# Performance work log

Measured on AMD Instinct MI355X. Metric: run time of the kernel, lower is better.

The kernel has to match this reference:

```python
import jax, jax.numpy as jnp
import numpy as np

B, C_IN, H, W = 2, 32, 512, 512
HIDDEN, SIZE = 768, 16
LATENT, NUM_CLASS = 128, 21
HP, WP = H // SIZE, W // SIZE
EPS = 1e-8
TEMP = 0.5


def setup_inputs() -> dict:
    key = jax.random.key(0)
    k1, k2, k3, k4, k5 = jax.random.split(key, 5)
    x = jax.random.normal(k1, (B, C_IN, H, W), dtype=jnp.float32)
    mask = jax.random.randint(k2, (B, NUM_CLASS, HP, WP), 0, 2).astype(jnp.int32)
    conv_w = jax.random.normal(k3, (HIDDEN, C_IN, SIZE, SIZE), dtype=jnp.float32) * 0.02
    conv_b = jax.random.normal(k4, (HIDDEN,), dtype=jnp.float32) * 0.02
    latent = jax.random.normal(k5, (1, LATENT * NUM_CLASS, HIDDEN), dtype=jnp.float32)
    return {"x": x, "mask": mask, "conv_w": conv_w, "conv_b": conv_b, "latent": latent}


def reference(x, mask, conv_w, conv_b, latent):
    # Patch embedding: Conv2d(kernel=stride=16) -> (B, HIDDEN, HP, WP)
    patch = jax.lax.conv_general_dilated(
        x, conv_w, window_strides=(SIZE, SIZE), padding='VALID',
        dimension_numbers=('NCHW', 'OIHW', 'NCHW'))
    patch = patch + conv_b[None, :, None, None]
    Bv = x.shape[0]
    N = HP * WP
    patch = patch.reshape(Bv, HIDDEN, N).transpose(0, 2, 1)  # (B, N, D)
    lat = jnp.broadcast_to(latent, (Bv, LATENT * NUM_CLASS, HIDDEN))  # (B, LC, D)

    # Cosine similarity as normalized batched matmul (same math as
    # torch CosineSimilarity over broadcast (B, LC, N, D))
    dots = jnp.einsum('bld,bnd->bln', lat, patch)  # (B, LC, N)
    lat_norm = jnp.linalg.norm(lat, axis=-1)       # (B, LC)
    pat_norm = jnp.linalg.norm(patch, axis=-1)     # (B, N)
    sim = dots / jnp.maximum(lat_norm[:, :, None] * pat_norm[:, None, :], EPS)

    sim = sim.reshape(Bv, LATENT, NUM_CLASS, HP, WP).mean(axis=1)  # (B, C, HP, WP)

    m = mask.astype(jnp.float32) >= 0.5
    s = jnp.sum(jnp.where(m, jnp.exp(sim / TEMP), 0.0))
    return -jnp.log(s)
```

## Files before the change

kernel.cpp:

```cpp
#include <hip/hip_runtime.h>
#include <hip/hip_bf16.h>
#include <math.h>

#define B_     2
#define CIN    32
#define HH     512
#define WW     512
#define HID    768
#define SZ     16
#define NPATCH 1024
#define KDIM   8192
#define NCLS   21
#define LAT    128
#define LC     2688
#define NP     (B_ * NPATCH)

typedef __attribute__((ext_vector_type(8))) short short8;
typedef __attribute__((ext_vector_type(4))) float f32x4;

__device__ __forceinline__ ushort f2bf(float f) {
    union { float f; unsigned u; } v; v.f = f;
    unsigned r = (v.u + 0x7fff + ((v.u >> 16) & 1)) >> 16;
    return (ushort)r;
}
__device__ __forceinline__ float bf2f(ushort u) {
    union { unsigned u; float f; } v; v.u = (unsigned)u << 16;
    return v.f;
}

__device__ __forceinline__ void gload16(const void* g, void* l) {
    __builtin_amdgcn_global_load_lds(
        (const __attribute__((address_space(1))) unsigned int*)g,
        (__attribute__((address_space(3))) unsigned int*)l, 16, 0, 0);
}

__global__ __launch_bounds__(256) void k_cvt_w(const float* __restrict__ w,
                                               ushort* __restrict__ wb) {
    size_t i = ((size_t)blockIdx.x * 256 + threadIdx.x) * 4;
    float4 v = *(const float4*)(w + i);
    ushort4 o;
    o.x = f2bf(v.x); o.y = f2bf(v.y); o.z = f2bf(v.z); o.w = f2bf(v.w);
    *(ushort4*)(wb + i) = o;
}

__global__ __launch_bounds__(256) void k_cvt_x(const float* __restrict__ x,
                                               ushort* __restrict__ xb) {
    int g = blockIdx.x * 256 + threadIdx.x;
    int w4 = g & 127;
    int h  = (g >> 7) & 511;
    int c  = (g >> 16) & 31;
    int b  = g >> 21;
    float4 v = *(const float4*)(x + (size_t)g * 4);
    int pw = w4 >> 2, j4 = w4 & 3;
    int ph = h >> 4,  i  = h & 15;
    size_t dst = ((size_t)((b << 10) | (ph << 5) | pw) << 13)
               + (c << 8) + (i << 4) + (j4 << 2);
    ushort4 o;
    o.x = f2bf(v.x); o.y = f2bf(v.y); o.z = f2bf(v.z); o.w = f2bf(v.w);
    *(ushort4*)(xb + dst) = o;
}

__global__ __launch_bounds__(256) void k_rowscale(const float* __restrict__ lat,
                                                  float* __restrict__ scale) {
    int wid  = blockIdx.x * 4 + (threadIdx.x >> 6);
    int lane = threadIdx.x & 63;
    const float* row = lat + (size_t)wid * HID;
    float s = 0.f;
#pragma unroll
    for (int q = 0; q < HID / 64; ++q) {
        float v = row[lane + q * 64];
        s += v * v;
    }
#pragma unroll
    for (int off = 32; off >= 1; off >>= 1) s += __shfl_xor(s, off, 64);
    if (lane == 0) scale[wid] = 1.0f / (128.0f * sqrtf(s));
}

__global__ __launch_bounds__(256) void k_classlat(const float* __restrict__ lat,
                                                  const float* __restrict__ scale,
                                                  float* __restrict__ classlat) {
    int cls = blockIdx.x;
    int t   = threadIdx.x;
    float a0 = 0.f, a1 = 0.f, a2 = 0.f;
#pragma unroll 4
    for (int u = 0; u < LAT; ++u) {
        int l = u * NCLS + cls;
        float sc = scale[l];
        const float* row = lat + (size_t)l * HID;
        a0 += row[t] * sc;
        a1 += row[t + 256] * sc;
        a2 += row[t + 512] * sc;
    }
    classlat[cls * HID + t]       = a0;
    classlat[cls * HID + t + 256] = a1;
    classlat[cls * HID + t + 512] = a2;
}

template <int SPLITK>
__global__ __launch_bounds__(256) void k_gemm(const ushort* __restrict__ xb,
                                              const ushort* __restrict__ wb,
                                              ushort* __restrict__ pbuf) {
    constexpr int KS = KDIM / SPLITK;
    __shared__ ushort Als[128 * 64];
    __shared__ ushort Bls[128 * 64];

    const int tid  = threadIdx.x;
    const int wv   = tid >> 6;
    const int lane = tid & 63;
    const int wm   = (wv >> 1) * 64;
    const int wn   = (wv & 1) * 64;

    const size_t abase = ((size_t)blockIdx.x * 128) * KDIM + (size_t)blockIdx.z * KS;
    const size_t bbase = ((size_t)blockIdx.y * 128) * KDIM + (size_t)blockIdx.z * KS;

    const int srow  = wv * 8 + (lane >> 3);
    const int skoff = (((lane & 7) ^ (lane >> 3)) * 8);

    f32x4 acc[4][4];
#pragma unroll
    for (int m = 0; m < 4; ++m)
#pragma unroll
        for (int n = 0; n < 4; ++n) acc[m][n] = (f32x4)(0.f);

    const int fr = lane & 15, fq = lane >> 4;
    const int frx = (fr & 7) * 8;

    for (int kk = 0; kk < KS; kk += 64) {
#pragma unroll
        for (int q = 0; q < 4; ++q) {
            const int row = q * 32 + srow;
            gload16(&xb[abase + (size_t)row * KDIM + kk + skoff], &Als[q * 2048 + wv * 512]);
            gload16(&wb[bbase + (size_t)row * KDIM + kk + skoff], &Bls[q * 2048 + wv * 512]);
        }
        __syncthreads();

#pragma unroll
        for (int s = 0; s < 2; ++s) {
            short8 af[4], bf[4];
#pragma unroll
            for (int m = 0; m < 4; ++m)
                af[m] = *(const short8*)&Als[(wm + m * 16 + fr) * 64 + ((s * 32 + fq * 8) ^ frx)];
#pragma unroll
            for (int n = 0; n < 4; ++n)
                bf[n] = *(const short8*)&Bls[(wn + n * 16 + fr) * 64 + ((s * 32 + fq * 8) ^ frx)];
#pragma unroll
            for (int m = 0; m < 4; ++m)
#pragma unroll
                for (int n = 0; n < 4; ++n)
                    acc[m][n] = __builtin_amdgcn_mfma_f32_16x16x32_bf16(af[m], bf[n], acc[m][n], 0, 0, 0);
        }
        __syncthreads();
    }

    ushort* outz = pbuf + (size_t)blockIdx.z * ((size_t)NP * HID);
#pragma unroll
    for (int m = 0; m < 4; ++m) {
#pragma unroll
        for (int n = 0; n < 4; ++n) {
            int col = blockIdx.y * 128 + wn + n * 16 + fr;
#pragma unroll
            for (int j = 0; j < 4; ++j) {
                int row = blockIdx.x * 128 + wm + m * 16 + fq * 4 + j;
                outz[(size_t)row * HID + col] = f2bf(acc[m][n][j]);
            }
        }
    }
}

template <int SPLITK>
__global__ __launch_bounds__(256) void k_final_partial(const ushort* __restrict__ pbuf,
                                                       const float* __restrict__ conv_b,
                                                       const float* __restrict__ classlat,
                                                       const int* __restrict__ mask,
                                                       float* __restrict__ partial) {
    const int p = blockIdx.x;
    const int b = p >> 10, n = p & 1023;
    const int t = threadIdx.x;
    const int lane = t & 63, wv = t >> 6;

    float f0 = conv_b[t], f1 = conv_b[t + 256], f2 = conv_b[t + 512];
    {
        const size_t base = (size_t)p * HID;
#pragma unroll
        for (int zz = 0; zz < SPLITK; ++zz) {
            const ushort* pz = pbuf + (size_t)zz * ((size_t)NP * HID) + base;
            f0 += bf2f(pz[t]);
            f1 += bf2f(pz[t + 256]);
            f2 += bf2f(pz[t + 512]);
        }
    }

    __shared__ float wsum[4];
    __shared__ float wdot[4][NCLS];
    __shared__ float cpart[NCLS];

    float ss = f0 * f0 + f1 * f1 + f2 * f2;
#pragma unroll
    for (int off = 32; off >= 1; off >>= 1) ss += __shfl_xor(ss, off, 64);
    if (lane == 0) wsum[wv] = ss;

    float dots[NCLS];
#pragma unroll
    for (int c = 0; c < NCLS; ++c) {
        const float* cl = classlat + c * HID;
        dots[c] = cl[t] * f0 + cl[t + 256] * f1 + cl[t + 512] * f2;
    }
#pragma unroll
    for (int c = 0; c < NCLS; ++c) {
        float v = dots[c];
#pragma unroll
        for (int off = 32; off >= 1; off >>= 1) v += __shfl_xor(v, off, 64);
        if (lane == 0) wdot[wv][c] = v;
    }
    __syncthreads();

    if (t < NCLS) {
        float tot  = wsum[0] + wsum[1] + wsum[2] + wsum[3];
        float invn = 1.0f / sqrtf(tot);
        float dot  = wdot[0][t] + wdot[1][t] + wdot[2][t] + wdot[3][t];
        float sim  = dot * invn;
        int   mv   = mask[(size_t)(b * NCLS + t) * NPATCH + n];
        cpart[t]   = (mv != 0) ? expf(sim * 2.0f) : 0.0f;
    }
    __syncthreads();
    if (t == 0) {
        float s = 0.f;
#pragma unroll
        for (int c = 0; c < NCLS; ++c) s += cpart[c];
        partial[p] = s;
    }
}

__global__ __launch_bounds__(256) void k_reduce(const float* __restrict__ partial,
                                                float* __restrict__ out) {
    int t = threadIdx.x;
    float s = 0.f;
    for (int i = t; i < NP; i += 256) s += partial[i];
#pragma unroll
    for (int off = 32; off >= 1; off >>= 1) s += __shfl_xor(s, off, 64);
    __shared__ float ws[4];
    if ((t & 63) == 0) ws[t >> 6] = s;
    __syncthreads();
    if (t == 0) out[0] = -logf(ws[0] + ws[1] + ws[2] + ws[3]);
}

extern "C" void kernel_launch(void* const* d_in, const int* in_sizes, int n_in,
                              void* d_out, int out_size, void* d_ws, size_t ws_size,
                              hipStream_t stream) {
    const float* x      = (const float*)d_in[0];
    const int*   mask   = (const int*)d_in[1];
    const float* conv_w = (const float*)d_in[2];
    const float* conv_b = (const float*)d_in[3];
    const float* latent = (const float*)d_in[4];
    float* out = (float*)d_out;

    const size_t xb_bytes   = (size_t)NP * KDIM * 2;
    const size_t wb_bytes   = (size_t)HID * KDIM * 2;
    const size_t pslice     = (size_t)NP * HID * 2;
    const size_t small_need = (size_t)NCLS * HID * 4 + LC * 4 + NP * 4 + 256;

    char* base = (char*)d_ws;
    ushort* xb   = (ushort*)base;
    ushort* wb   = (ushort*)(base + xb_bytes);
    ushort* pbuf = (ushort*)(base + xb_bytes + wb_bytes);

    int splitk = 1;
    const size_t fixed = xb_bytes + wb_bytes + small_need;
    if (ws_size >= fixed + 8 * pslice)      splitk = 8;
    else if (ws_size >= fixed + 4 * pslice) splitk = 4;
    else if (ws_size >= fixed + 2 * pslice) splitk = 2;

    float* classlat = (float*)(base + xb_bytes + wb_bytes + (size_t)splitk * pslice);
    float* scale    = classlat + NCLS * HID;
    float* partial  = scale + LC;

    k_cvt_w<<<HID * KDIM / 4 / 256, 256, 0, stream>>>(conv_w, wb);
    k_cvt_x<<<B_ * CIN * HH * WW / 4 / 256, 256, 0, stream>>>(x, xb);
    k_rowscale<<<LC / 4, 256, 0, stream>>>(latent, scale);
    k_classlat<<<NCLS, 256, 0, stream>>>(latent, scale, classlat);

    dim3 g(NP / 128, HID / 128, splitk);
    switch (splitk) {
        case 8: k_gemm<8><<<g, 256, 0, stream>>>(xb, wb, pbuf); break;
        case 4: k_gemm<4><<<g, 256, 0, stream>>>(xb, wb, pbuf); break;
        case 2: k_gemm<2><<<g, 256, 0, stream>>>(xb, wb, pbuf); break;
        default: k_gemm<1><<<g, 256, 0, stream>>>(xb, wb, pbuf); break;
    }

    switch (splitk) {
        case 8: k_final_partial<8><<<NP, 256, 0, stream>>>(pbuf, conv_b, classlat, mask, partial); break;
        case 4: k_final_partial<4><<<NP, 256, 0, stream>>>(pbuf, conv_b, classlat, mask, partial); break;
        case 2: k_final_partial<2><<<NP, 256, 0, stream>>>(pbuf, conv_b, classlat, mask, partial); break;
        default: k_final_partial<1><<<NP, 256, 0, stream>>>(pbuf, conv_b, classlat, mask, partial); break;
    }
    k_reduce<<<1, 256, 0, stream>>>(partial, out);
}
```

Baseline: 99.32 us.

## Fuse prep kernels, remap GEMM workgroups per XCD, fold final reduction via atomics

Merges the four preprocessing kernels (weight cast, x patch cast, latent row-norm scaling, class latent averaging) into one launch. The x conversion now iterates in destination order, so writes are contiguous and reads are gathered. Remaps GEMM workgroup ids so that neighbouring tiles land on the same XCD for better L2 reuse. Replaces the separate reduce kernel with atomic accumulation and a last-block-finishes pattern, which saves launches but makes the float summation order nondeterministic.

```diff
diff --git a/kernel.cpp b/kernel.cpp
--- a/kernel.cpp
+++ b/kernel.cpp
@@ -1,5 +1,4 @@
 #include <hip/hip_runtime.h>
-#include <hip/hip_bf16.h>
 #include <math.h>
 
 #define B_     2
@@ -15,6 +14,9 @@
 #define LC     2688
 #define NP     (B_ * NPATCH)
 
+#define NB_W   6144
+#define NB_X   16384
+
 typedef __attribute__((ext_vector_type(8))) short short8;
 typedef __attribute__((ext_vector_type(4))) float f32x4;
 
@@ -34,66 +36,78 @@
         (__attribute__((address_space(3))) unsigned int*)l, 16, 0, 0);
 }
 
-__global__ __launch_bounds__(256) void k_cvt_w(const float* __restrict__ w,
-                                               ushort* __restrict__ wb) {
-    size_t i = ((size_t)blockIdx.x * 256 + threadIdx.x) * 4;
-    float4 v = *(const float4*)(w + i);
-    ushort4 o;
-    o.x = f2bf(v.x); o.y = f2bf(v.y); o.z = f2bf(v.z); o.w = f2bf(v.w);
-    *(ushort4*)(wb + i) = o;
-}
-
-__global__ __launch_bounds__(256) void k_cvt_x(const float* __restrict__ x,
-                                               ushort* __restrict__ xb) {
-    int g = blockIdx.x * 256 + threadIdx.x;
-    int w4 = g & 127;
-    int h  = (g >> 7) & 511;
-    int c  = (g >> 16) & 31;
-    int b  = g >> 21;
-    float4 v = *(const float4*)(x + (size_t)g * 4);
-    int pw = w4 >> 2, j4 = w4 & 3;
-    int ph = h >> 4,  i  = h & 15;
-    size_t dst = ((size_t)((b << 10) | (ph << 5) | pw) << 13)
-               + (c << 8) + (i << 4) + (j4 << 2);
-    ushort4 o;
-    o.x = f2bf(v.x); o.y = f2bf(v.y); o.z = f2bf(v.z); o.w = f2bf(v.w);
-    *(ushort4*)(xb + dst) = o;
-}
-
-__global__ __launch_bounds__(256) void k_rowscale(const float* __restrict__ lat,
-                                                  float* __restrict__ scale) {
-    int wid  = blockIdx.x * 4 + (threadIdx.x >> 6);
-    int lane = threadIdx.x & 63;
-    const float* row = lat + (size_t)wid * HID;
-    float s = 0.f;
-#pragma unroll
-    for (int q = 0; q < HID / 64; ++q) {
-        float v = row[lane + q * 64];
-        s += v * v;
-    }
-#pragma unroll
-    for (int off = 32; off >= 1; off >>= 1) s += __shfl_xor(s, off, 64);
-    if (lane == 0) scale[wid] = 1.0f / (128.0f * sqrtf(s));
-}
-
-__global__ __launch_bounds__(256) void k_classlat(const float* __restrict__ lat,
-                                                  const float* __restrict__ scale,
-                                                  float* __restrict__ classlat) {
-    int cls = blockIdx.x;
-    int t   = threadIdx.x;
-    float a0 = 0.f, a1 = 0.f, a2 = 0.f;
+__global__ __launch_bounds__(256) void k_prep(const float* __restrict__ w,
+                                              const float* __restrict__ x,
+                                              const float* __restrict__ lat,
+                                              ushort* __restrict__ wb,
+                                              ushort* __restrict__ xb,
+                                              float* __restrict__ classlat,
+                                              float* __restrict__ gsum,
+                                              unsigned* __restrict__ gcnt) {
+    const int bid = blockIdx.x;
+    const int t   = threadIdx.x;
+
+    if (bid < NB_W) {
+        size_t i = ((size_t)bid * 256 + t) * 4;
+        float4 v = *(const float4*)(w + i);
+        ushort4 o;
+        o.x = f2bf(v.x); o.y = f2bf(v.y); o.z = f2bf(v.z); o.w = f2bf(v.w);
+        *(ushort4*)(wb + i) = o;
+    } else if (bid < NB_W + NB_X) {
+        int e  = (bid - NB_W) * 256 + t;
+        int p  = e >> 11;
+        int o4 = e & 2047;
+        int c  = o4 >> 6;
+        int i  = (o4 >> 2) & 15;
+        int j0 = (o4 & 3) << 2;
+        int b  = p >> 10, ph = (p >> 5) & 31, pw = p & 31;
+        size_t src = (((size_t)(b * CIN + c) * HH + ph * 16 + i) * WW) + pw * 16 + j0;
+        float4 v = *(const float4*)(x + src);
+        ushort4 o;
+        o.x = f2bf(v.x); o.y = f2bf(v.y); o.z = f2bf(v.z); o.w = f2bf(v.w);
+        *(ushort4*)(xb + (size_t)e * 4) = o;
+    } else if (bid < NB_W + NB_X + NCLS) {
+        const int cls  = bid - (NB_W + NB_X);
+        const int lane = t & 63, wv = t >> 6;
+        __shared__ float sc_sh[LAT];
+
+        for (int q = 0; q < 32; q += 2) {
+            int u0 = wv * 32 + q;
+            const float* r0 = lat + (size_t)(u0 * NCLS + cls) * HID;
+            const float* r1 = lat + (size_t)((u0 + 1) * NCLS + cls) * HID;
+            float s0 = 0.f, s1 = 0.f;
+#pragma unroll
+            for (int e = 0; e < HID / 64; ++e) {
+                float a = r0[lane + e * 64]; s0 += a * a;
+                float b = r1[lane + e * 64]; s1 += b * b;
+            }
+#pragma unroll
+            for (int off = 32; off >= 1; off >>= 1) {
+                s0 += __shfl_xor(s0, off, 64);
+                s1 += __shfl_xor(s1, off, 64);
+            }
+            if (lane == 0) {
+                sc_sh[u0]     = 1.0f / (128.0f * sqrtf(s0));
+                sc_sh[u0 + 1] = 1.0f / (128.0f * sqrtf(s1));
+            }
+        }
+        __syncthreads();
+
+        float a0 = 0.f, a1 = 0.f, a2 = 0.f;
 #pragma unroll 4
-    for (int u = 0; u < LAT; ++u) {
-        int l = u * NCLS + cls;
-        float sc = scale[l];
-        const float* row = lat + (size_t)l * HID;
-        a0 += row[t] * sc;
-        a1 += row[t + 256] * sc;
-        a2 += row[t + 512] * sc;
-    }
-    classlat[cls * HID + t]       = a0;
-    classlat[cls * HID + t + 256] = a1;
-    classlat[cls * HID + t + 512] = a2;
+        for (int u = 0; u < LAT; ++u) {
+            float sc = sc_sh[u];
+            const float* row = lat + (size_t)(u * NCLS + cls) * HID;
+            a0 += row[t] * sc;
+            a1 += row[t + 256] * sc;
+            a2 += row[t + 512] * sc;
+        }
+        classlat[cls * HID + t]       = a0;
+        classlat[cls * HID + t + 256] = a1;
+        classlat[cls * HID + t + 512] = a2;
+    } else {
+        if (t == 0) { *gsum = 0.0f; *gcnt = 0u; }
+    }
 }
 
 template <int SPLITK>
@@ -104,14 +118,22 @@
     __shared__ ushort Als[128 * 64];
     __shared__ ushort Bls[128 * 64];
 
+    const int flat = blockIdx.x + 16 * (blockIdx.y + 6 * blockIdx.z);
+    constexpr int nwg = 96 * SPLITK;
+    const int wg = (flat & 7) * (nwg >> 3) + (flat >> 3);
+    const int bz = wg / 96;
+    const int rr = wg - bz * 96;
+    const int by = rr % 6;
+    const int bx = rr / 6;
+
     const int tid  = threadIdx.x;
     const int wv   = tid >> 6;
     const int lane = tid & 63;
     const int wm   = (wv >> 1) * 64;
     const int wn   = (wv & 1) * 64;
 
-    const size_t abase = ((size_t)blockIdx.x * 128) * KDIM + (size_t)blockIdx.z * KS;
-    const size_t bbase = ((size_t)blockIdx.y * 128) * KDIM + (size_t)blockIdx.z * KS;
+    const size_t abase = ((size_t)bx * 128) * KDIM + (size_t)bz * KS;
+    const size_t bbase = ((size_t)by * 128) * KDIM + (size_t)bz * KS;
 
     const int srow  = wv * 8 + (lane >> 3);
     const int skoff = (((lane & 7) ^ (lane >> 3)) * 8);
@@ -152,15 +174,15 @@
         __syncthreads();
     }
 
-    ushort* outz = pbuf + (size_t)blockIdx.z * ((size_t)NP * HID);
+    ushort* outz = pbuf + (size_t)bz * ((size_t)NP * HID);
 #pragma unroll
     for (int m = 0; m < 4; ++m) {
 #pragma unroll
         for (int n = 0; n < 4; ++n) {
-            int col = blockIdx.y * 128 + wn + n * 16 + fr;
+            int col = by * 128 + wn + n * 16 + fr;
 #pragma unroll
             for (int j = 0; j < 4; ++j) {
-                int row = blockIdx.x * 128 + wm + m * 16 + fq * 4 + j;
+                int row = bx * 128 + wm + m * 16 + fq * 4 + j;
                 outz[(size_t)row * HID + col] = f2bf(acc[m][n][j]);
             }
         }
@@ -168,11 +190,13 @@
 }
 
 template <int SPLITK>
-__global__ __launch_bounds__(256) void k_final_partial(const ushort* __restrict__ pbuf,
-                                                       const float* __restrict__ conv_b,
-                                                       const float* __restrict__ classlat,
-                                                       const int* __restrict__ mask,
-                                                       float* __restrict__ partial) {
+__global__ __launch_bounds__(256) void k_final(const ushort* __restrict__ pbuf,
+                                               const float* __restrict__ conv_b,
+                                               const float* __restrict__ classlat,
+                                               const int* __restrict__ mask,
+                                               float* __restrict__ gsum,
+                                               unsigned* __restrict__ gcnt,
+                                               float* __restrict__ out) {
     const int p = blockIdx.x;
     const int b = p >> 10, n = p & 1023;
     const int t = threadIdx.x;
@@ -227,21 +251,13 @@
         float s = 0.f;
 #pragma unroll
         for (int c = 0; c < NCLS; ++c) s += cpart[c];
-        partial[p] = s;
-    }
-}
-
-__global__ __launch_bounds__(256) void k_reduce(const float* __restrict__ partial,
-                                                float* __restrict__ out) {
-    int t = threadIdx.x;
-    float s = 0.f;
-    for (int i = t; i < NP; i += 256) s += partial[i];
-#pragma unroll
-    for (int off = 32; off >= 1; off >>= 1) s += __shfl_xor(s, off, 64);
-    __shared__ float ws[4];
-    if ((t & 63) == 0) ws[t >> 6] = s;
-    __syncthreads();
-    if (t == 0) out[0] = -logf(ws[0] + ws[1] + ws[2] + ws[3]);
+        atomicAdd(gsum, s);
+        __threadfence();
+        unsigned prev = atomicAdd(gcnt, 1u);
+        if (prev == NP - 1) {
+            out[0] = -logf(atomicAdd(gsum, 0.0f));
+        }
+    }
 }
 
 extern "C" void kernel_launch(void* const* d_in, const int* in_sizes, int n_in,
@@ -257,7 +273,7 @@
     const size_t xb_bytes   = (size_t)NP * KDIM * 2;
     const size_t wb_bytes   = (size_t)HID * KDIM * 2;
     const size_t pslice     = (size_t)NP * HID * 2;
-    const size_t small_need = (size_t)NCLS * HID * 4 + LC * 4 + NP * 4 + 256;
+    const size_t small_need = (size_t)NCLS * HID * 4 + 256;
 
     char* base = (char*)d_ws;
     ushort* xb   = (ushort*)base;
@@ -270,14 +286,12 @@
     else if (ws_size >= fixed + 4 * pslice) splitk = 4;
     else if (ws_size >= fixed + 2 * pslice) splitk = 2;
 
-    float* classlat = (float*)(base + xb_bytes + wb_bytes + (size_t)splitk * pslice);
-    float* scale    = classlat + NCLS * HID;
-    float* partial  = scale + LC;
-
-    k_cvt_w<<<HID * KDIM / 4 / 256, 256, 0, stream>>>(conv_w, wb);
-    k_cvt_x<<<B_ * CIN * HH * WW / 4 / 256, 256, 0, stream>>>(x, xb);
-    k_rowscale<<<LC / 4, 256, 0, stream>>>(latent, scale);
-    k_classlat<<<NCLS, 256, 0, stream>>>(latent, scale, classlat);
+    float*    classlat = (float*)(base + xb_bytes + wb_bytes + (size_t)splitk * pslice);
+    float*    gsum     = classlat + NCLS * HID;
+    unsigned* gcnt     = (unsigned*)(gsum + 1);
+
+    k_prep<<<NB_W + NB_X + NCLS + 1, 256, 0, stream>>>(conv_w, x, latent, wb, xb,
+                                                       classlat, gsum, gcnt);
 
     dim3 g(NP / 128, HID / 128, splitk);
     switch (splitk) {
@@ -288,10 +302,9 @@
     }
 
     switch (splitk) {
-        case 8: k_final_partial<8><<<NP, 256, 0, stream>>>(pbuf, conv_b, classlat, mask, partial); break;
-        case 4: k_final_partial<4><<<NP, 256, 0, stream>>>(pbuf, conv_b, classlat, mask, partial); break;
-        case 2: k_final_partial<2><<<NP, 256, 0, stream>>>(pbuf, conv_b, classlat, mask, partial); break;
-        default: k_final_partial<1><<<NP, 256, 0, stream>>>(pbuf, conv_b, classlat, mask, partial); break;
-    }
-    k_reduce<<<1, 256, 0, stream>>>(partial, out);
-}
+        case 8: k_final<8><<<NP, 256, 0, stream>>>(pbuf, conv_b, classlat, mask, gsum, gcnt, out); break;
+        case 4: k_final<4><<<NP, 256, 0, stream>>>(pbuf, conv_b, classlat, mask, gsum, gcnt, out); break;
+        case 2: k_final<2><<<NP, 256, 0, stream>>>(pbuf, conv_b, classlat, mask, gsum, gcnt, out); break;
+        default: k_final<1><<<NP, 256, 0, stream>>>(pbuf, conv_b, classlat, mask, gsum, gcnt, out); break;
+    }
+}
```

After: 144.1 us. +45.0%, slower.
